# Kernel tuning notes

Hardware: AMD Instinct MI355X
Metric: run time of the kernel (lower is better)

Reference implementation:

```python
import jax, jax.numpy as jnp
import numpy as np
from jax import lax

LATENT = 64
NUM_EMB = 512
BETA = 0.25
DN = ('NCHW', 'OIHW', 'NCHW')


def conv(x, w, b, stride, pad):
    y = lax.conv_general_dilated(x, w, (stride, stride), [(pad, pad), (pad, pad)],
                                 dimension_numbers=DN)
    return y + b[None, :, None, None]


def tconv(x, w, b, stride, pad, opad):
    # torch ConvTranspose2d(k=3, stride, padding=pad, output_padding=opad)
    # == dilated conv with lhs_dilation=stride, padding (k-1-pad, k-1-pad+opad),
    #    spatially-flipped kernel. w is stored OIHW (out, in, kh, kw).
    k = w.shape[2]
    lo, hi = k - 1 - pad, k - 1 - pad + opad
    y = lax.conv_general_dilated(x, w[:, :, ::-1, ::-1], (1, 1), [(lo, hi), (lo, hi)],
                                 lhs_dilation=(stride, stride), dimension_numbers=DN)
    return y + b[None, :, None, None]


def vector_quantize(z, codebook):
    # z: (B, D, H, W); codebook: (K, D)
    B, D, H, W = z.shape
    flat = z.transpose(0, 2, 3, 1).reshape(-1, D)  # (BHW, D)
    d = (jnp.sum(flat ** 2, axis=1, keepdims=True)
         + jnp.sum(codebook ** 2, axis=1)
         - 2.0 * flat @ codebook.T)  # (BHW, K)
    idx = jnp.argmin(d, axis=1)
    q = codebook[idx].reshape(B, H, W, D).transpose(0, 3, 1, 2)  # (B, D, H, W)
    commitment = jnp.mean((lax.stop_gradient(q) - z) ** 2)
    codebook_loss = jnp.mean((q - lax.stop_gradient(z)) ** 2)
    loss = BETA * commitment + codebook_loss
    q_ste = z + lax.stop_gradient(q - z)  # straight-through estimator
    return q_ste, loss


def setup_inputs() -> dict:
    key = jax.random.key(0)
    ks = jax.random.split(key, 16)
    f32 = jnp.float32
    inp = {
        'x': jax.random.uniform(ks[0], (1024, 1, 50, 50), dtype=f32),
        'enc_w1': jax.random.normal(ks[1], (32, 1, 3, 3), f32) * 0.1,
        'enc_b1': jnp.zeros((32,), f32),
        'enc_w2': jax.random.normal(ks[2], (64, 32, 3, 3), f32) * 0.05,
        'enc_b2': jnp.zeros((64,), f32),
        'enc_w3': jax.random.normal(ks[3], (LATENT, 64, 1, 1), f32) * 0.1,
        'enc_b3': jnp.zeros((LATENT,), f32),
        'codebook': jax.random.uniform(ks[4], (NUM_EMB, LATENT), dtype=f32),
        'dec_w1': jax.random.normal(ks[5], (64, LATENT, 3, 3), f32) * 0.05,
        'dec_b1': jnp.zeros((64,), f32),
        'dec_w2': jax.random.normal(ks[6], (32, 64, 3, 3), f32) * 0.05,
        'dec_b2': jnp.zeros((32,), f32),
        'dec_w3': jax.random.normal(ks[7], (1, 32, 3, 3), f32) * 0.05,
        'dec_b3': jnp.zeros((1,), f32),
    }
    return inp


def reference(x, enc_w1, enc_b1, enc_w2, enc_b2, enc_w3, enc_b3, codebook,
              dec_w1, dec_b1, dec_w2, dec_b2, dec_w3, dec_b3):
    # encoder: (B,1,50,50) -> (B,LATENT,13,13)
    h = jax.nn.relu(conv(x, enc_w1, enc_b1, 2, 1))
    h = jax.nn.relu(conv(h, enc_w2, enc_b2, 2, 1))
    z = conv(h, enc_w3, enc_b3, 1, 0)
    q, vq_loss = vector_quantize(z, codebook)
    # decoder: 13 -> 25 -> 50
    h = jax.nn.relu(tconv(q, dec_w1, dec_b1, 2, 1, 0))
    h = jax.nn.relu(tconv(h, dec_w2, dec_b2, 2, 1, 1))
    x_recon = jax.nn.sigmoid(conv(h, dec_w3, dec_b3, 1, 1))
    return x_recon, vq_loss
```

## Files before the change

kernel.cpp:

```cpp
#include <hip/hip_runtime.h>
#include <math.h>


typedef __attribute__((ext_vector_type(8))) short s8v;
typedef __attribute__((ext_vector_type(4))) float f4v;
typedef __attribute__((ext_vector_type(4))) int i4v;
typedef __attribute__((ext_vector_type(4))) short s4v;

__device__ inline unsigned short f2bf(float f) {
    unsigned u = __builtin_bit_cast(unsigned, f);
    return (unsigned short)((u + 0x7fffu + ((u >> 16) & 1u)) >> 16);
}
__device__ inline float bf2f(unsigned short h) {
    return __builtin_bit_cast(float, ((unsigned)h) << 16);
}

__global__ __launch_bounds__(256) void k_prep_all(
        const float* __restrict__ cb,  const float* __restrict__ ew2,
        const float* __restrict__ ew3, const float* __restrict__ dw1,
        const float* __restrict__ dw2,
        unsigned short* __restrict__ cbm, unsigned short* __restrict__ wB2n,
        unsigned short* __restrict__ wB1, unsigned short* __restrict__ wB2,
        unsigned short* __restrict__ wB3, float* __restrict__ cn,
        float* __restrict__ loss) {
    int i = blockIdx.x * 256 + threadIdx.x;
    if (i < 98304) {
        int j = i & 7, lane = (i >> 3) & 63;
        int kc = (i >> 9) % 6, nt = (i >> 9) / 6;
        int n = nt * 16 + (lane & 15);
        int k = kc * 32 + ((lane >> 4) << 3) + j;
        int seg = k >> 6, kk = k & 63;
        float c = cb[n * 64 + kk];
        unsigned short ch = f2bf(c);
        cbm[i] = (seg == 1) ? f2bf(c - bf2f(ch)) : ch;
    } else if (i < 153600) {
        int q = i - 98304;
        int j = q & 7, lane = (q >> 3) & 63;
        int kc = (q >> 9) % 27, nt = (q >> 9) / 27;
        int k = kc * 32 + ((lane >> 4) << 3) + j;
        int co = nt * 16 + (lane & 15);
        int part = (k < 288) ? 0 : (k < 576) ? 1 : 0;
        int kk = (k < 288) ? k : (k < 576) ? k - 288 : k - 576;
        int tap = kk >> 5, ci = kk & 31;
        float v = ew2[(co * 32 + ci) * 9 + tap];
        unsigned short hi = f2bf(v);
        wB2n[q] = part ? f2bf(v - bf2f(hi)) : hi;
    } else if (i < 219136) {
        int q = i - 153600;
        int j = q & 7, l = (q >> 3) & 63, kc = (q >> 9) & 7, nt = q >> 12;
        int n = nt * 16 + (l & 15), k = kc * 32 + (l >> 4) * 8 + j;
        int cls = n >> 6, co = n & 63, p = k >> 6, ci = k & 63;
        int jh = -1, jw = -1;
        if (cls == 0)      { if (p == 0) { jh = 1; jw = 1; } }
        else if (cls == 1) { if (p == 1) { jh = 1; jw = 0; } else if (p == 0) { jh = 1; jw = 2; } }
        else if (cls == 2) { if (p == 2) { jh = 0; jw = 1; } else if (p == 0) { jh = 2; jw = 1; } }
        else { if (p == 3) { jh = 0; jw = 0; } else if (p == 2) { jh = 0; jw = 2; }
               else if (p == 1) { jh = 2; jw = 0; } else { jh = 2; jw = 2; } }
        float v = (jh >= 0) ? dw1[((co * 64 + ci) * 3 + jh) * 3 + jw] : 0.f;
        wB1[q] = f2bf(v);
    } else if (i < 251904) {
        int q = i - 219136;
        int j = q & 7, l = (q >> 3) & 63, kc = (q >> 9) & 7, nt = q >> 12;
        int n = nt * 16 + (l & 15), k = kc * 32 + (l >> 4) * 8 + j;
        int cls = n >> 5, co = n & 31, p = k >> 6, ci = k & 63;
        int jh = -1, jw = -1;
        if (cls == 0)      { if (p == 0) { jh = 1; jw = 1; } }
        else if (cls == 1) { if (p == 1) { jh = 1; jw = 0; } else if (p == 0) { jh = 1; jw = 2; } }
        else if (cls == 2) { if (p == 2) { jh = 0; jw = 1; } else if (p == 0) { jh = 2; jw = 1; } }
        else { if (p == 3) { jh = 0; jw = 0; } else if (p == 2) { jh = 0; jw = 2; }
               else if (p == 1) { jh = 2; jw = 0; } else { jh = 2; jw = 2; } }
        float v = (jh >= 0) ? dw2[((co * 64 + ci) * 3 + jh) * 3 + jw] : 0.f;
        wB2[q] = f2bf(v);
    } else if (i < 264192) {
        int q = i - 251904;
        int j = q & 7, lane = (q >> 3) & 63;
        int kc = (q >> 9) % 6, nt = (q >> 9) / 6;
        int k = kc * 32 + ((lane >> 4) << 3) + j;
        int n = nt * 16 + (lane & 15);
        int part = (k < 64) ? 0 : (k < 128) ? 1 : 0;
        int kk = (k < 64) ? k : (k < 128) ? k - 64 : k - 128;
        float v = ew3[n * 64 + kk];
        unsigned short hi = f2bf(v);
        wB3[q] = part ? f2bf(v - bf2f(hi)) : hi;
    } else if (i < 264704) {
        int k = i - 264192;
        const float* r = cb + k * 64;
        float s = 0.f;
#pragma unroll
        for (int c = 0; c < 64; ++c) s += r[c] * r[c];
        cn[k] = s;
    } else if (i == 264704) {
        *loss = 0.f;
    }
}

__global__ __launch_bounds__(256) void k_conv1(const float* __restrict__ x,
                                               const float* __restrict__ w,
                                               const float* __restrict__ b,
                                               unsigned short* __restrict__ h1,
                                               int total) {
    __shared__ float4 wl4[72];
    float* wl = (float*)wl4;
    int tid = threadIdx.x;
    for (int t = tid; t < 288; t += 256) {
        int tap = t >> 5, co = t & 31;
        wl[t] = w[co * 9 + tap];
    }
    __syncthreads();
    int pix = blockIdx.x * 256 + tid;
    if (pix >= total) return;
    int n = pix / 625, p = pix % 625, oh = p / 25, ow = p % 25;
    const float* xp = x + (size_t)n * 2500;
    float4 a[8];
#pragma unroll
    for (int j = 0; j < 8; ++j) a[j] = ((const float4*)b)[j];
#pragma unroll
    for (int kh = 0; kh < 3; ++kh) {
        int ih = 2 * oh - 1 + kh;
        if ((unsigned)ih >= 50u) continue;
#pragma unroll
        for (int kw = 0; kw < 3; ++kw) {
            int iw = 2 * ow - 1 + kw;
            if ((unsigned)iw >= 50u) continue;
            float v = xp[ih * 50 + iw];
            int tap = kh * 3 + kw;
#pragma unroll
            for (int j = 0; j < 8; ++j) {
                float4 ww = wl4[tap * 8 + j];
                a[j].x += v * ww.x; a[j].y += v * ww.y;
                a[j].z += v * ww.z; a[j].w += v * ww.w;
            }
        }
    }
    unsigned short hi[32], lo[32];
#pragma unroll
    for (int j = 0; j < 8; ++j) {
        float vv[4] = {a[j].x, a[j].y, a[j].z, a[j].w};
#pragma unroll
        for (int e = 0; e < 4; ++e) {
            float v = fmaxf(vv[e], 0.f);
            unsigned short h = f2bf(v);
            hi[j * 4 + e] = h;
            lo[j * 4 + e] = f2bf(v - bf2f(h));
        }
    }
    i4v* op = (i4v*)(h1 + (size_t)pix * 64);
#pragma unroll
    for (int g = 0; g < 4; ++g) {
        i4v ph, pl;
#pragma unroll
        for (int e = 0; e < 4; ++e) {
            int b0 = g * 8 + e * 2;
            ph[e] = (int)((unsigned)hi[b0] | ((unsigned)hi[b0 + 1] << 16));
            pl[e] = (int)((unsigned)lo[b0] | ((unsigned)lo[b0 + 1] << 16));
        }
        op[g] = ph;
        op[4 + g] = pl;
    }
}

__global__ __launch_bounds__(256) void k_enc_m(const unsigned short* __restrict__ h1,
                                               const unsigned short* __restrict__ B2n,
                                               const unsigned short* __restrict__ B3,
                                               const float* __restrict__ b2,
                                               const float* __restrict__ b3,
                                               unsigned short* __restrict__ z, int npix) {
    __shared__ short a1[16 * 872];
    __shared__ short a2[16 * 200];
    __shared__ short czs[16 * 136];
    int tid = threadIdx.x, blk = blockIdx.x;
    {
        int m = tid >> 4, chunk = tid & 15;
        if (chunk < 9) {
            int pix = blk * 16 + m;
            i4v vh[4], vl[4];
#pragma unroll
            for (int g = 0; g < 4; ++g) {
                vh[g] = (i4v){0, 0, 0, 0};
                vl[g] = (i4v){0, 0, 0, 0};
            }
            if (pix < npix) {
                int n = pix / 169, p = pix % 169, oh = p / 13, ow = p % 13;
                int kh = chunk / 3, kw = chunk % 3;
                int ih = 2 * oh - 1 + kh, iw = 2 * ow - 1 + kw;
                if (((unsigned)ih < 25u) && ((unsigned)iw < 25u)) {
                    const i4v* ip = (const i4v*)(h1 + (((size_t)n * 25 + ih) * 25 + iw) * 64);
#pragma unroll
                    for (int g = 0; g < 4; ++g) { vh[g] = ip[g]; vl[g] = ip[4 + g]; }
                }
            }
            short* row = a1 + m * 872 + chunk * 32;
            i4v* d0 = (i4v*)row;
            i4v* d1 = (i4v*)(row + 288);
            i4v* d2 = (i4v*)(row + 576);
#pragma unroll
            for (int g = 0; g < 4; ++g) { d0[g] = vh[g]; d1[g] = vh[g]; d2[g] = vl[g]; }
        }
    }
    __syncthreads();
    int wave = tid >> 6, lane = tid & 63;
    int arow1 = (lane & 15) * 872 + (lane >> 4) * 8;
    f4v acc = (f4v){0.f, 0.f, 0.f, 0.f};
#pragma unroll
    for (int kc = 0; kc < 27; ++kc) {
        s8v a = *(const s8v*)(a1 + arow1 + kc * 32);
        s8v b = *(const s8v*)((const short*)B2n + ((size_t)((wave * 27 + kc) * 64 + lane)) * 8);
        acc = __builtin_amdgcn_mfma_f32_16x16x32_bf16(a, b, acc, 0, 0, 0);
    }
    {
        float bv = b2[wave * 16 + (lane & 15)];
        int n = wave * 16 + (lane & 15);
#pragma unroll
        for (int r = 0; r < 4; ++r) {
            int m = (lane >> 4) * 4 + r;
            float h = fmaxf(acc[r] + bv, 0.f);
            unsigned short hh = f2bf(h);
            unsigned short ll = f2bf(h - bf2f(hh));
            a2[m * 200 + n] = (short)hh;
            a2[m * 200 + 64 + n] = (short)hh;
            a2[m * 200 + 128 + n] = (short)ll;
        }
    }
    __syncthreads();
    int arow2 = (lane & 15) * 200 + (lane >> 4) * 8;
    f4v acc2 = (f4v){0.f, 0.f, 0.f, 0.f};
#pragma unroll
    for (int kc = 0; kc < 6; ++kc) {
        s8v a = *(const s8v*)(a2 + arow2 + kc * 32);
        s8v b = *(const s8v*)((const short*)B3 + ((size_t)((wave * 6 + kc) * 64 + lane)) * 8);
        acc2 = __builtin_amdgcn_mfma_f32_16x16x32_bf16(a, b, acc2, 0, 0, 0);
    }
    {
        float bv = b3[wave * 16 + (lane & 15)];
        int n = wave * 16 + (lane & 15);
#pragma unroll
        for (int r = 0; r < 4; ++r) {
            int m = (lane >> 4) * 4 + r;
            float v = acc2[r] + bv;
            unsigned short hh = f2bf(v);
            czs[m * 136 + n] = (short)hh;
            czs[m * 136 + 64 + n] = (short)f2bf(v - bf2f(hh));
        }
    }
    __syncthreads();
    {
        int m = tid >> 4, t = tid & 15;
        int pix = blk * 16 + m;
        if (pix < npix)
            *(i4v*)(z + (size_t)pix * 128 + t * 8) = *(i4v*)(czs + m * 136 + t * 8);
    }
}

__global__ __launch_bounds__(256) void k_vq_m(const unsigned short* __restrict__ z,
                                              const float* __restrict__ cb,
                                              const unsigned short* __restrict__ cbm,
                                              const float* __restrict__ cn,
                                              unsigned short* __restrict__ q,
                                              float* __restrict__ loss, int npix) {
    __shared__ short a_lds[32 * 200];
    __shared__ float reds[4 * 32];
    __shared__ int   redk[4 * 32];
    __shared__ int   bkf[32];
    __shared__ float lred[4];
    int tid = threadIdx.x, blk = blockIdx.x;
    {
        int m = tid >> 3, p = tid & 7;
        int pix = blk * 32 + m;
        i4v vh = (i4v){0, 0, 0, 0};
        i4v vl = (i4v){0, 0, 0, 0};
        if (pix < npix) {
            const i4v* src = (const i4v*)(z + (size_t)pix * 128);
            vh = src[p];
            vl = src[8 + p];
        }
        short* row = a_lds + m * 200;
        *(i4v*)(row + p * 8) = vh;
        *(i4v*)(row + 64 + p * 8) = vh;
        *(i4v*)(row + 128 + p * 8) = vl;
    }
    __syncthreads();
    int wave = tid >> 6, lane = tid & 63;
    s8v af[2][6];
#pragma unroll
    for (int mt = 0; mt < 2; ++mt) {
        int arow = (mt * 16 + (lane & 15)) * 200 + (lane >> 4) * 8;
#pragma unroll
        for (int kc = 0; kc < 6; ++kc)
            af[mt][kc] = *(const s8v*)(a_lds + arow + kc * 32);
    }
    float bd[2][4];
    int bk[2][4];
#pragma unroll
    for (int mt = 0; mt < 2; ++mt)
#pragma unroll
        for (int r = 0; r < 4; ++r) { bd[mt][r] = 3.4e38f; bk[mt][r] = 0; }
#pragma unroll 2
    for (int nt = 0; nt < 8; ++nt) {
        int ntg = wave * 8 + nt;
        s8v bf[6];
#pragma unroll
        for (int kc = 0; kc < 6; ++kc)
            bf[kc] = *(const s8v*)((const short*)cbm + ((size_t)((ntg * 6 + kc) * 64 + lane)) * 8);
        f4v acc0 = (f4v){0.f, 0.f, 0.f, 0.f};
        f4v acc1 = (f4v){0.f, 0.f, 0.f, 0.f};
#pragma unroll
        for (int kc = 0; kc < 6; ++kc) {
            acc0 = __builtin_amdgcn_mfma_f32_16x16x32_bf16(af[0][kc], bf[kc], acc0, 0, 0, 0);
            acc1 = __builtin_amdgcn_mfma_f32_16x16x32_bf16(af[1][kc], bf[kc], acc1, 0, 0, 0);
        }
        int kcol = ntg * 16 + (lane & 15);
        float cnk = cn[kcol];
#pragma unroll
        for (int r = 0; r < 4; ++r) {
            float d0 = cnk - 2.f * acc0[r];
            if (d0 < bd[0][r]) { bd[0][r] = d0; bk[0][r] = kcol; }
            float d1 = cnk - 2.f * acc1[r];
            if (d1 < bd[1][r]) { bd[1][r] = d1; bk[1][r] = kcol; }
        }
    }
#pragma unroll
    for (int off = 1; off < 16; off <<= 1) {
#pragma unroll
        for (int mt = 0; mt < 2; ++mt)
#pragma unroll
            for (int r = 0; r < 4; ++r) {
                float od = __shfl_xor(bd[mt][r], off);
                int ok = __shfl_xor(bk[mt][r], off);
                if (od < bd[mt][r] || (od == bd[mt][r] && ok < bk[mt][r])) {
                    bd[mt][r] = od; bk[mt][r] = ok;
                }
            }
    }
    if ((lane & 15) == 0) {
#pragma unroll
        for (int mt = 0; mt < 2; ++mt)
#pragma unroll
            for (int r = 0; r < 4; ++r) {
                int m = mt * 16 + (lane >> 4) * 4 + r;
                reds[wave * 32 + m] = bd[mt][r];
                redk[wave * 32 + m] = bk[mt][r];
            }
    }
    __syncthreads();
    if (tid < 32) {
        float d0 = reds[tid]; int k0 = redk[tid];
#pragma unroll
        for (int w = 1; w < 4; ++w) {
            float dw = reds[w * 32 + tid]; int kw = redk[w * 32 + tid];
            if (dw < d0 || (dw == d0 && kw < k0)) { d0 = dw; k0 = kw; }
        }
        bkf[tid] = k0;
    }
    __syncthreads();
    float lsum = 0.f;
#pragma unroll
    for (int it = 0; it < 2; ++it) {
        int m = tid >> 3, c4 = (tid & 7) + it * 8;
        int pix = blk * 32 + m;
        if (pix < npix) {
            int k0 = bkf[m];
            float4 cq = ((const float4*)cb)[(size_t)k0 * 16 + c4];
            const short* rz = a_lds + m * 200 + c4 * 4;
            s4v zh4 = *(const s4v*)rz;
            s4v zl4 = *(const s4v*)(rz + 128);
            float zx = bf2f((unsigned short)zh4[0]) + bf2f((unsigned short)zl4[0]);
            float zy = bf2f((unsigned short)zh4[1]) + bf2f((unsigned short)zl4[1]);
            float zz = bf2f((unsigned short)zh4[2]) + bf2f((unsigned short)zl4[2]);
            float zw = bf2f((unsigned short)zh4[3]) + bf2f((unsigned short)zl4[3]);
            float dx = cq.x - zx, dy = cq.y - zy, dz = cq.z - zz, dw = cq.w - zw;
            lsum += dx * dx + dy * dy + dz * dz + dw * dw;
            s4v qs;
            qs[0] = (short)f2bf(cq.x); qs[1] = (short)f2bf(cq.y);
            qs[2] = (short)f2bf(cq.z); qs[3] = (short)f2bf(cq.w);
            *(s4v*)(q + (size_t)pix * 64 + c4 * 4) = qs;
        }
    }
#pragma unroll
    for (int off = 32; off > 0; off >>= 1) lsum += __shfl_down(lsum, off);
    if ((tid & 63) == 0) lred[tid >> 6] = lsum;
    __syncthreads();
    if (tid == 0) {
        float t = lred[0] + lred[1] + lred[2] + lred[3];
        atomicAdd(loss, t * (1.25f / 11075584.f));
    }
}

__global__ __launch_bounds__(256) void k_tconv1_m(const unsigned short* __restrict__ q,
                                                  const unsigned short* __restrict__ wB,
                                                  const float* __restrict__ bias,
                                                  unsigned short* __restrict__ d1,
                                                  int nquad) {
    __shared__ short a_lds[32 * 264];
    __shared__ short c_lds[32 * 264];
    int tid = threadIdx.x, blk = blockIdx.x;
#pragma unroll
    for (int pass = 0; pass < 4; ++pass) {
        int idx = tid + pass * 256;
        int m = idx >> 5, sub = idx & 31;
        int qg = blk * 32 + m;
        int p = sub >> 3, ci0 = (sub & 7) * 8;
        i4v v = (i4v){0, 0, 0, 0};
        if (qg < nquad) {
            int img = qg / 169, r = qg % 169, qm = r / 13, qw = r % 13;
            int sm = qm + (p >> 1), sw = qw + (p & 1);
            if (sm < 13 && sw < 13)
                v = *(const i4v*)(q + (((size_t)img * 13 + sm) * 13 + sw) * 64 + ci0);
        }
        *(i4v*)(a_lds + m * 264 + sub * 8) = v;
    }
    __syncthreads();
    int wave = tid >> 6, lane = tid & 63;
    f4v acc[2][4];
#pragma unroll
    for (int mt = 0; mt < 2; ++mt)
#pragma unroll
        for (int i = 0; i < 4; ++i) acc[mt][i] = (f4v){0.f, 0.f, 0.f, 0.f};
    float bv[4];
#pragma unroll
    for (int i = 0; i < 4; ++i) bv[i] = bias[((wave * 4 + i) * 16 + (lane & 15)) & 63];
#pragma unroll
    for (int kc = 0; kc < 8; ++kc) {
        s8v a0 = *(const s8v*)(a_lds + ((lane & 15)) * 264 + (lane >> 4) * 8 + kc * 32);
        s8v a1 = *(const s8v*)(a_lds + (16 + (lane & 15)) * 264 + (lane >> 4) * 8 + kc * 32);
#pragma unroll
        for (int i = 0; i < 4; ++i) {
            int nt = wave * 4 + i;
            s8v b = *(const s8v*)((const short*)wB + ((size_t)((nt * 8 + kc) * 64 + lane)) * 8);
            acc[0][i] = __builtin_amdgcn_mfma_f32_16x16x32_bf16(a0, b, acc[0][i], 0, 0, 0);
            acc[1][i] = __builtin_amdgcn_mfma_f32_16x16x32_bf16(a1, b, acc[1][i], 0, 0, 0);
        }
    }
#pragma unroll
    for (int mt = 0; mt < 2; ++mt)
#pragma unroll
        for (int i = 0; i < 4; ++i) {
            int n = (wave * 4 + i) * 16 + (lane & 15);
#pragma unroll
            for (int r2 = 0; r2 < 4; ++r2) {
                int m = mt * 16 + (lane >> 4) * 4 + r2;
                float v = fmaxf(acc[mt][i][r2] + bv[i], 0.f);
                c_lds[m * 264 + n] = (short)f2bf(v);
            }
        }
    __syncthreads();
#pragma unroll
    for (int pass = 0; pass < 4; ++pass) {
        int ch = tid + pass * 256;
        int m = ch >> 5, cpart = ch & 31;
        int qg = blk * 32 + m;
        if (qg >= nquad) continue;
        int img = qg / 169, r = qg % 169, qm = r / 13, qw = r % 13;
        int cls = cpart >> 3, co8 = (cpart & 7) * 8;
        int oh = 2 * qm + (cls >> 1), ow = 2 * qw + (cls & 1);
        if (oh >= 25 || ow >= 25) continue;
        i4v val = *(i4v*)(c_lds + m * 264 + cls * 64 + co8);
        *(i4v*)(d1 + (((size_t)img * 25 + oh) * 25 + ow) * 64 + co8) = val;
    }
}

__global__ __launch_bounds__(256) void k_tconv2_m(const unsigned short* __restrict__ d1,
                                                  const unsigned short* __restrict__ wB,
                                                  const float* __restrict__ bias,
                                                  unsigned short* __restrict__ d2,
                                                  int nquad) {
    __shared__ short a_lds[32 * 264];
    __shared__ short c_lds[32 * 136];
    int tid = threadIdx.x, blk = blockIdx.x;
#pragma unroll
    for (int pass = 0; pass < 4; ++pass) {
        int idx = tid + pass * 256;
        int m = idx >> 5, sub = idx & 31;
        int qg = blk * 32 + m;
        int p = sub >> 3, ci0 = (sub & 7) * 8;
        i4v v = (i4v){0, 0, 0, 0};
        if (qg < nquad) {
            int img = qg / 625, r = qg % 625, qm = r / 25, qw = r % 25;
            int sm = qm + (p >> 1), sw = qw + (p & 1);
            if (sm < 25 && sw < 25)
                v = *(const i4v*)(d1 + (((size_t)img * 25 + sm) * 25 + sw) * 64 + ci0);
        }
        *(i4v*)(a_lds + m * 264 + sub * 8) = v;
    }
    __syncthreads();
    int wave = tid >> 6, lane = tid & 63;
    f4v acc[2][2];
#pragma unroll
    for (int mt = 0; mt < 2; ++mt)
#pragma unroll
        for (int i = 0; i < 2; ++i) acc[mt][i] = (f4v){0.f, 0.f, 0.f, 0.f};
    float bv[2];
#pragma unroll
    for (int i = 0; i < 2; ++i) bv[i] = bias[((wave * 2 + i) * 16 + (lane & 15)) & 31];
#pragma unroll
    for (int kc = 0; kc < 8; ++kc) {
        s8v a0 = *(const s8v*)(a_lds + ((lane & 15)) * 264 + (lane >> 4) * 8 + kc * 32);
        s8v a1 = *(const s8v*)(a_lds + (16 + (lane & 15)) * 264 + (lane >> 4) * 8 + kc * 32);
#pragma unroll
        for (int i = 0; i < 2; ++i) {
            int nt = wave * 2 + i;
            s8v b = *(const s8v*)((const short*)wB + ((size_t)((nt * 8 + kc) * 64 + lane)) * 8);
            acc[0][i] = __builtin_amdgcn_mfma_f32_16x16x32_bf16(a0, b, acc[0][i], 0, 0, 0);
            acc[1][i] = __builtin_amdgcn_mfma_f32_16x16x32_bf16(a1, b, acc[1][i], 0, 0, 0);
        }
    }
#pragma unroll
    for (int mt = 0; mt < 2; ++mt)
#pragma unroll
        for (int i = 0; i < 2; ++i) {
            int n = (wave * 2 + i) * 16 + (lane & 15);
#pragma unroll
            for (int r2 = 0; r2 < 4; ++r2) {
                int m = mt * 16 + (lane >> 4) * 4 + r2;
                float v = fmaxf(acc[mt][i][r2] + bv[i], 0.f);
                c_lds[m * 136 + n] = (short)f2bf(v);
            }
        }
    __syncthreads();
#pragma unroll
    for (int pass = 0; pass < 2; ++pass) {
        int ch = tid + pass * 256;
        int m = ch >> 4, cpart = ch & 15;
        int qg = blk * 32 + m;
        if (qg >= nquad) continue;
        int img = qg / 625, r = qg % 625, qm = r / 25, qw = r % 25;
        int cls = cpart >> 2, co8 = (cpart & 3) * 8;
        int oh = 2 * qm + (cls >> 1), ow = 2 * qw + (cls & 1);
        i4v val = *(i4v*)(c_lds + m * 136 + cls * 32 + co8);
        *(i4v*)(d2 + (((size_t)img * 50 + oh) * 50 + ow) * 32 + co8) = val;
    }
}

__global__ __launch_bounds__(256) void k_convf(const unsigned short* __restrict__ in,
                                               const float* __restrict__ w,
                                               const float* __restrict__ b,
                                               float* __restrict__ out, int total) {
    __shared__ float wl[288];
    int tid = threadIdx.x;
    for (int t = tid; t < 288; t += 256) {
        int tap = t >> 5, ci = t & 31;
        wl[t] = w[ci * 9 + tap];
    }
    __syncthreads();
    int pix = blockIdx.x * 256 + tid;
    if (pix >= total) return;
    int n = pix / 2500, p = pix % 2500, oh = p / 50, ow = p % 50;
    float acc = b[0];
#pragma unroll
    for (int kh = 0; kh < 3; ++kh) {
        int ih = oh - 1 + kh;
        if ((unsigned)ih >= 50u) continue;
#pragma unroll
        for (int kw = 0; kw < 3; ++kw) {
            int iw = ow - 1 + kw;
            if ((unsigned)iw >= 50u) continue;
            const float* wt = wl + (kh * 3 + kw) * 32;
            const i4v* ip4 = (const i4v*)(in + (((size_t)n * 50 + ih) * 50 + iw) * 32);
#pragma unroll
            for (int c8 = 0; c8 < 4; ++c8) {
                i4v u = ip4[c8];
#pragma unroll
                for (int e = 0; e < 4; ++e) {
                    unsigned uu = (unsigned)u[e];
                    float x0 = __builtin_bit_cast(float, uu << 16);
                    float x1 = __builtin_bit_cast(float, uu & 0xffff0000u);
                    acc = fmaf(x0, wt[c8 * 8 + e * 2], acc);
                    acc = fmaf(x1, wt[c8 * 8 + e * 2 + 1], acc);
                }
            }
        }
    }
    out[pix] = 1.f / (1.f + expf(-acc));
}

extern "C" void kernel_launch(void* const* d_in, const int* in_sizes, int n_in,
                              void* d_out, int out_size, void* d_ws, size_t ws_size,
                              hipStream_t stream) {
    const float* x   = (const float*)d_in[0];
    const float* ew1 = (const float*)d_in[1];
    const float* eb1 = (const float*)d_in[2];
    const float* ew2 = (const float*)d_in[3];
    const float* eb2 = (const float*)d_in[4];
    const float* ew3 = (const float*)d_in[5];
    const float* eb3 = (const float*)d_in[6];
    const float* cb  = (const float*)d_in[7];
    const float* dw1 = (const float*)d_in[8];
    const float* db1 = (const float*)d_in[9];
    const float* dw2 = (const float*)d_in[10];
    const float* db2 = (const float*)d_in[11];
    const float* dw3 = (const float*)d_in[12];
    const float* db3 = (const float*)d_in[13];
    float* out = (float*)d_out;
    float* loss = out + 2560000;

    float* ws = (float*)d_ws;
    float* cn = ws;
    unsigned short* wB1  = (unsigned short*)(ws + 512);
    unsigned short* wB2  = (unsigned short*)(ws + 33280);
    unsigned short* wB2n = (unsigned short*)(ws + 49664);
    unsigned short* wB3  = (unsigned short*)(ws + 77312);
    unsigned short* cbm  = (unsigned short*)(ws + 83456);
    const size_t tw_floats = 132608;

    const int B = 1024;
    const size_t A_per = 40000, B_per = 20000;
    size_t avail = (ws_size / 4 > tw_floats) ? ws_size / 4 - tw_floats : 0;
    int BC = (int)(avail / (A_per + B_per));
    if (BC > B) BC = B;
    if (BC < 1) BC = 1;
    float* regA = ws + tw_floats;
    float* regB = regA + (size_t)BC * A_per;

    k_prep_all<<<1035, 256, 0, stream>>>(cb, ew2, ew3, dw1, dw2,
                                         cbm, wB2n, wB1, wB2, wB3, cn, loss);

    for (int n0 = 0; n0 < B; n0 += BC) {
        int bc = (B - n0 < BC) ? (B - n0) : BC;
        const float* xch = x + (size_t)n0 * 2500;

        int t1 = bc * 625;
        unsigned short* h1p = (unsigned short*)regA;
        k_conv1<<<(t1 + 255) / 256, 256, 0, stream>>>(xch, ew1, eb1, h1p, t1);

        int npix = bc * 169;
        unsigned short* zp = (unsigned short*)regB;
        k_enc_m<<<(npix + 15) / 16, 256, 0, stream>>>(h1p, wB2n, wB3, eb2, eb3, zp, npix);

        unsigned short* qb = (unsigned short*)regA;
        k_vq_m<<<(npix + 31) / 32, 256, 0, stream>>>(zp, cb, cbm, cn, qb, loss, npix);

        unsigned short* d1 = (unsigned short*)regB;
        k_tconv1_m<<<(npix + 31) / 32, 256, 0, stream>>>(qb, wB1, db1, d1, npix);

        int nq2 = bc * 625;
        unsigned short* d2 = (unsigned short*)regA;
        k_tconv2_m<<<(nq2 + 31) / 32, 256, 0, stream>>>(d1, wB2, db2, d2, nq2);

        int t6 = bc * 2500;
        k_convf<<<(t6 + 255) / 256, 256, 0, stream>>>(d2, dw3, db3, out + (size_t)n0 * 2500, t6);
    }
}
```

Before: 495.5 us.

## Restructure VQ kernel so each wave scans full codebook for its own pixels

The VQ argmin kernel now processes 128 pixels per block, with each wave owning 32 pixels and scanning all 512 codes, instead of 32 pixels per block with the codebook split across waves. This removes the cross-wave LDS reduction and one barrier. The duplicated hi copy in LDS is dropped by reusing A fragments in the MFMA sequence. The trade-off is that each wave now reads the full bf16 codebook fragments, so codebook traffic per pixel is the same but spread over fewer blocks, which lowers parallelism. Loss accumulation now does one atomic per wave.

```diff
diff --git a/kernel.cpp b/kernel.cpp
--- a/kernel.cpp
+++ b/kernel.cpp
@@ -257,36 +257,30 @@
                                               const float* __restrict__ cn,
                                               unsigned short* __restrict__ q,
                                               float* __restrict__ loss, int npix) {
-    __shared__ short a_lds[32 * 200];
-    __shared__ float reds[4 * 32];
-    __shared__ int   redk[4 * 32];
-    __shared__ int   bkf[32];
-    __shared__ float lred[4];
+    __shared__ short a_lds[128 * 136];
+    __shared__ int bkf[128];
     int tid = threadIdx.x, blk = blockIdx.x;
     {
-        int m = tid >> 3, p = tid & 7;
-        int pix = blk * 32 + m;
-        i4v vh = (i4v){0, 0, 0, 0};
-        i4v vl = (i4v){0, 0, 0, 0};
-        if (pix < npix) {
-            const i4v* src = (const i4v*)(z + (size_t)pix * 128);
-            vh = src[p];
-            vl = src[8 + p];
-        }
-        short* row = a_lds + m * 200;
-        *(i4v*)(row + p * 8) = vh;
-        *(i4v*)(row + 64 + p * 8) = vh;
-        *(i4v*)(row + 128 + p * 8) = vl;
+        const i4v* src = (const i4v*)(z + (size_t)blk * 128 * 128);
+#pragma unroll
+        for (int it = 0; it < 8; ++it) {
+            int L = it * 256 + tid;
+            int m = L >> 4, s = L & 15;
+            int pix = blk * 128 + m;
+            i4v v = (i4v){0, 0, 0, 0};
+            if (pix < npix) v = src[L];
+            *(i4v*)(a_lds + m * 136 + s * 8) = v;
+        }
     }
     __syncthreads();
     int wave = tid >> 6, lane = tid & 63;
-    s8v af[2][6];
+    s8v af[2][4];
 #pragma unroll
     for (int mt = 0; mt < 2; ++mt) {
-        int arow = (mt * 16 + (lane & 15)) * 200 + (lane >> 4) * 8;
-#pragma unroll
-        for (int kc = 0; kc < 6; ++kc)
-            af[mt][kc] = *(const s8v*)(a_lds + arow + kc * 32);
+        int arow = (wave * 32 + mt * 16 + (lane & 15)) * 136 + (lane >> 4) * 8;
+#pragma unroll
+        for (int kcd = 0; kcd < 4; ++kcd)
+            af[mt][kcd] = *(const s8v*)(a_lds + arow + kcd * 32);
     }
     float bd[2][4];
     int bk[2][4];
@@ -295,20 +289,26 @@
 #pragma unroll
         for (int r = 0; r < 4; ++r) { bd[mt][r] = 3.4e38f; bk[mt][r] = 0; }
 #pragma unroll 2
-    for (int nt = 0; nt < 8; ++nt) {
-        int ntg = wave * 8 + nt;
+    for (int nt = 0; nt < 32; ++nt) {
         s8v bf[6];
 #pragma unroll
         for (int kc = 0; kc < 6; ++kc)
-            bf[kc] = *(const s8v*)((const short*)cbm + ((size_t)((ntg * 6 + kc) * 64 + lane)) * 8);
+            bf[kc] = *(const s8v*)((const short*)cbm + ((size_t)((nt * 6 + kc) * 64 + lane)) * 8);
         f4v acc0 = (f4v){0.f, 0.f, 0.f, 0.f};
         f4v acc1 = (f4v){0.f, 0.f, 0.f, 0.f};
-#pragma unroll
-        for (int kc = 0; kc < 6; ++kc) {
-            acc0 = __builtin_amdgcn_mfma_f32_16x16x32_bf16(af[0][kc], bf[kc], acc0, 0, 0, 0);
-            acc1 = __builtin_amdgcn_mfma_f32_16x16x32_bf16(af[1][kc], bf[kc], acc1, 0, 0, 0);
-        }
-        int kcol = ntg * 16 + (lane & 15);
+        acc0 = __builtin_amdgcn_mfma_f32_16x16x32_bf16(af[0][0], bf[0], acc0, 0, 0, 0);
+        acc1 = __builtin_amdgcn_mfma_f32_16x16x32_bf16(af[1][0], bf[0], acc1, 0, 0, 0);
+        acc0 = __builtin_amdgcn_mfma_f32_16x16x32_bf16(af[0][1], bf[1], acc0, 0, 0, 0);
+        acc1 = __builtin_amdgcn_mfma_f32_16x16x32_bf16(af[1][1], bf[1], acc1, 0, 0, 0);
+        acc0 = __builtin_amdgcn_mfma_f32_16x16x32_bf16(af[0][0], bf[2], acc0, 0, 0, 0);
+        acc1 = __builtin_amdgcn_mfma_f32_16x16x32_bf16(af[1][0], bf[2], acc1, 0, 0, 0);
+        acc0 = __builtin_amdgcn_mfma_f32_16x16x32_bf16(af[0][1], bf[3], acc0, 0, 0, 0);
+        acc1 = __builtin_amdgcn_mfma_f32_16x16x32_bf16(af[1][1], bf[3], acc1, 0, 0, 0);
+        acc0 = __builtin_amdgcn_mfma_f32_16x16x32_bf16(af[0][2], bf[4], acc0, 0, 0, 0);
+        acc1 = __builtin_amdgcn_mfma_f32_16x16x32_bf16(af[1][2], bf[4], acc1, 0, 0, 0);
+        acc0 = __builtin_amdgcn_mfma_f32_16x16x32_bf16(af[0][3], bf[5], acc0, 0, 0, 0);
+        acc1 = __builtin_amdgcn_mfma_f32_16x16x32_bf16(af[1][3], bf[5], acc1, 0, 0, 0);
+        int kcol = nt * 16 + (lane & 15);
         float cnk = cn[kcol];
 #pragma unroll
         for (int r = 0; r < 4; ++r) {
@@ -335,34 +335,22 @@
 #pragma unroll
         for (int mt = 0; mt < 2; ++mt)
 #pragma unroll
-            for (int r = 0; r < 4; ++r) {
-                int m = mt * 16 + (lane >> 4) * 4 + r;
-                reds[wave * 32 + m] = bd[mt][r];
-                redk[wave * 32 + m] = bk[mt][r];
-            }
-    }
-    __syncthreads();
-    if (tid < 32) {
-        float d0 = reds[tid]; int k0 = redk[tid];
-#pragma unroll
-        for (int w = 1; w < 4; ++w) {
-            float dw = reds[w * 32 + tid]; int kw = redk[w * 32 + tid];
-            if (dw < d0 || (dw == d0 && kw < k0)) { d0 = dw; k0 = kw; }
-        }
-        bkf[tid] = k0;
+            for (int r = 0; r < 4; ++r)
+                bkf[wave * 32 + mt * 16 + (lane >> 4) * 4 + r] = bk[mt][r];
     }
     __syncthreads();
     float lsum = 0.f;
 #pragma unroll
-    for (int it = 0; it < 2; ++it) {
-        int m = tid >> 3, c4 = (tid & 7) + it * 8;
-        int pix = blk * 32 + m;
+    for (int it = 0; it < 8; ++it) {
+        int L = it * 256 + tid;
+        int m = L >> 4, c4 = L & 15;
+        int pix = blk * 128 + m;
         if (pix < npix) {
             int k0 = bkf[m];
             float4 cq = ((const float4*)cb)[(size_t)k0 * 16 + c4];
-            const short* rz = a_lds + m * 200 + c4 * 4;
+            const short* rz = a_lds + m * 136 + c4 * 4;
             s4v zh4 = *(const s4v*)rz;
-            s4v zl4 = *(const s4v*)(rz + 128);
+            s4v zl4 = *(const s4v*)(rz + 64);
             float zx = bf2f((unsigned short)zh4[0]) + bf2f((unsigned short)zl4[0]);
             float zy = bf2f((unsigned short)zh4[1]) + bf2f((unsigned short)zl4[1]);
             float zz = bf2f((unsigned short)zh4[2]) + bf2f((unsigned short)zl4[2]);
@@ -377,12 +365,7 @@
     }
 #pragma unroll
     for (int off = 32; off > 0; off >>= 1) lsum += __shfl_down(lsum, off);
-    if ((tid & 63) == 0) lred[tid >> 6] = lsum;
-    __syncthreads();
-    if (tid == 0) {
-        float t = lred[0] + lred[1] + lred[2] + lred[3];
-        atomicAdd(loss, t * (1.25f / 11075584.f));
-    }
+    if (lane == 0) atomicAdd(loss, lsum * (1.25f / 11075584.f));
 }
 
 __global__ __launch_bounds__(256) void k_tconv1_m(const unsigned short* __restrict__ q,
@@ -626,7 +609,7 @@
         k_enc_m<<<(npix + 15) / 16, 256, 0, stream>>>(h1p, wB2n, wB3, eb2, eb3, zp, npix);
 
         unsigned short* qb = (unsigned short*)regA;
-        k_vq_m<<<(npix + 31) / 32, 256, 0, stream>>>(zp, cb, cbm, cn, qb, loss, npix);
+        k_vq_m<<<(npix + 127) / 128, 256, 0, stream>>>(zp, cb, cbm, cn, qb, loss, npix);
 
         unsigned short* d1 = (unsigned short*)regB;
         k_tconv1_m<<<(npix + 31) / 32, 256, 0, stream>>>(qb, wB1, db1, d1, npix);
```

Result: slower. 522.4 us (+5.4%).
